# Optimization experiments

Measured on AMD Instinct MI355X. Metric: run time of the kernel, lower is better.

## Reference

```python
import jax, jax.numpy as jnp
import numpy as np
from jax import lax

# fixed finite-difference kernels (HWIO)
KXN = jnp.asarray([[0., -1., 1.]], dtype=jnp.float32).reshape(1, 3, 1, 1)
KXP = jnp.asarray([[-1., 1., 0.]], dtype=jnp.float32).reshape(1, 3, 1, 1)
KYN = jnp.asarray([[1.], [-1.], [0.]], dtype=jnp.float32).reshape(3, 1, 1, 1)
KYP = jnp.asarray([[0.], [1.], [-1.]], dtype=jnp.float32).reshape(3, 1, 1, 1)


def conv2d(x, k):
    # NHWC input, HWIO kernel, SAME padding, stride 1
    return lax.conv_general_dilated(x, k, (1, 1), 'SAME',
                                    dimension_numbers=('NHWC', 'HWIO', 'NHWC'))


def setup_inputs() -> dict:
    key = jax.random.key(0)
    ks = jax.random.split(key, 11)
    B, H, W = 8, 512, 512
    return {
        'u': jax.random.normal(ks[0], (B, H, W, 1), jnp.float32),
        'image': jax.random.uniform(ks[1], (B, H, W, 1), jnp.float32),
        'conv_kernel_x': jax.random.normal(ks[2], (3, 3, 1, 32), jnp.float32) * 0.05,
        'conv_kernel_y': jax.random.normal(ks[3], (3, 3, 1, 32), jnp.float32) * 0.05,
        'sep_kernel_depthwise': jax.random.normal(ks[4], (3, 3, 1, 8), jnp.float32) * 0.05,
        'sep_kernel_pointwise': jax.random.normal(ks[5], (1, 1, 8, 8), jnp.float32) * 0.05,
        'conv_kernel_curve_0': jax.random.normal(ks[6], (5, 5, 1, 8), jnp.float32) * 0.05,
        'conv_kernel_curve_1': jax.random.normal(ks[7], (5, 5, 8, 8), jnp.float32) * 0.05,
        'conv_kernel_curve_2': jax.random.normal(ks[8], (3, 3, 8, 16), jnp.float32) * 0.05,
        'conv_kernel_smoother': jax.random.normal(ks[9], (5, 5, 1, 1), jnp.float32) * 0.05,
        'kappa_kernel': jax.random.normal(ks[10], (H, W, 1), jnp.float32) * 0.05,
    }


def reference(u, image, conv_kernel_x, conv_kernel_y, sep_kernel_depthwise,
              sep_kernel_pointwise, conv_kernel_curve_0, conv_kernel_curve_1,
              conv_kernel_curve_2, conv_kernel_smoother, kappa_kernel):
    # separable conv on the (fixed) image: in_ch=1 so depthwise == standard conv
    edges = conv2d(conv2d(image, sep_kernel_depthwise), sep_kernel_pointwise)
    edges = jnp.sum(jax.nn.relu(edges), axis=-1, keepdims=True)
    edges = jax.nn.soft_sign(edges)  # x / (1 + |x|)

    grad_edges_x = jnp.sum(jax.nn.relu(conv2d(edges, conv_kernel_x)), axis=-1, keepdims=True)
    grad_edges_y = jnp.sum(jax.nn.relu(conv2d(edges, conv_kernel_y)), axis=-1, keepdims=True)

    xp = conv2d(u, KXP)
    xn = conv2d(u, KXN)
    yp = conv2d(u, KYP)
    yn = conv2d(u, KYN)

    fxp = jax.nn.relu(grad_edges_x)
    fxn = -jax.nn.relu(-grad_edges_x)
    fyp = jax.nn.relu(grad_edges_y)
    fyn = -jax.nn.relu(-grad_edges_y)

    kappa = conv2d(conv2d(conv2d(u, conv_kernel_curve_0), conv_kernel_curve_1), conv_kernel_curve_2)
    kappa = jnp.sum(kappa, axis=-1, keepdims=True)
    kappa = kappa * kappa_kernel  # (H,W,1) broadcasts over batch
    kappa = conv2d(kappa, conv_kernel_smoother)

    return u + fxp * xp + fxn * xn + fyp * yp + fyn * yn + edges + kappa
```

## Files before the change

### kernel.cpp

```cpp
#include <hip/hip_runtime.h>
#include <cstddef>

#define HH 512
#define WW 512
#define BB 8
#define T  32

#define F0    256
#define KT0   1280
#define WS_NEEDED_BYTES ((size_t)4096 * 4)

typedef __attribute__((ext_vector_type(8))) short short8;
typedef __attribute__((ext_vector_type(4))) float float4v;

__device__ inline unsigned short f2bf(float f) {
  unsigned u = __builtin_bit_cast(unsigned, f);
  unsigned r = (u + 0x7FFFu + ((u >> 16) & 1u)) >> 16;
  return (unsigned short)r;
}
__device__ inline float bf2f(unsigned short h) {
  unsigned u = ((unsigned)h) << 16;
  return __builtin_bit_cast(float, u);
}

__global__ __launch_bounds__(256) void precompute_kernels(
    const float* __restrict__ kd,
    const float* __restrict__ kp,
    const float* __restrict__ k0,
    const float* __restrict__ k1,
    const float* __restrict__ k2,
    const float* __restrict__ kx,
    const float* __restrict__ ky,
    float* __restrict__ ws) {
  __shared__ float k9[648];
  __shared__ float k2s[72];
  __shared__ float kef[121];
  const int tid = threadIdx.x;

  for (int idx = tid; idx < 72; idx += 256) {
    int c = idx & 7, pq = idx >> 3;
    float s = 0.f;
    for (int c0 = 0; c0 < 8; ++c0) s = fmaf(kd[pq * 8 + c0], kp[c0 * 8 + c], s);
    ws[idx] = s;
  }
  for (int idx = tid; idx < 72; idx += 256) {
    int c1 = idx & 7, tv = idx >> 3;
    float s = 0.f;
    for (int c2 = 0; c2 < 16; ++c2) s += k2[(tv * 8 + c1) * 16 + c2];
    k2s[idx] = s;
  }
  for (int idx = tid; idx < 648; idx += 256) {
    int c1 = idx & 7;
    int ab = idx >> 3;
    int a = ab / 9, b = ab % 9;
    float s = 0.f;
    int plo = a > 4 ? a - 4 : 0, phi = a < 4 ? a : 4;
    int qlo = b > 4 ? b - 4 : 0, qhi = b < 4 ? b : 4;
    for (int p = plo; p <= phi; ++p)
      for (int q = qlo; q <= qhi; ++q) {
        int r = a - p, sx = b - q;
        const float* k0p = &k0[(p * 5 + q) * 8];
        const float* k1p = &k1[((r * 5 + sx) * 8) * 8 + c1];
        for (int c0 = 0; c0 < 8; ++c0) s = fmaf(k0p[c0], k1p[c0 * 8], s);
      }
    k9[idx] = s;
  }
  for (int idx = tid; idx < 2048; idx += 256) {
    int nt = idx >> 9, ln = (idx >> 3) & 63, j = idx & 7;
    int k = (ln >> 4) * 8 + j;
    int n = nt * 16 + (ln & 15);
    float v = 0.f;
    if (k < 9) v = (n < 32) ? kx[k * 32 + n] : ky[k * 32 + (n - 32)];
    ((unsigned short*)ws)[F0 * 2 + idx] = f2bf(v);
  }
  __syncthreads();
  for (int idx = tid; idx < 121; idx += 256) {
    int A = idx / 11, B = idx % 11;
    float s = 0.f;
    int tlo = A > 8 ? A - 8 : 0, thi = A < 2 ? A : 2;
    int vlo = B > 8 ? B - 8 : 0, vhi = B < 2 ? B : 2;
    for (int t = tlo; t <= thi; ++t)
      for (int v = vlo; v <= vhi; ++v) {
        int a = A - t, b = B - v;
        for (int c1 = 0; c1 < 8; ++c1)
          s = fmaf(k9[(a * 9 + b) * 8 + c1], k2s[(t * 3 + v) * 8 + c1], s);
      }
    ws[72 + idx] = s;
    kef[idx] = s;
  }
  __syncthreads();
  for (int idx = tid; idx < 5632; idx += 256) {
    int b = idx >> 9, ln = (idx >> 3) & 63, j = idx & 7;
    int m = ln & 15;
    int k = (ln >> 4) * 8 + j;
    int a = k - m - 3;
    float v = ((unsigned)a < 11u) ? kef[a * 11 + b] : 0.f;
    ((unsigned short*)ws)[KT0 * 2 + idx] = f2bf(v);
  }
}

__global__ __launch_bounds__(256) void fused(
    const float* __restrict__ u, const float* __restrict__ img,
    const float* __restrict__ kk, const float* __restrict__ sm,
    const float* __restrict__ ws, float* __restrict__ out) {
  __shared__ unsigned short suT[58 * 72];
  __shared__ float si[36 * 36];
  __shared__ unsigned short sebf[34 * 36];
  __shared__ float skp[36 * 37];
  __shared__ float sgx[32 * 32];
  __shared__ float sgy[32 * 32];

  const int bx = blockIdx.x * T, by = blockIdx.y * T, b = blockIdx.z;
  const int tid = threadIdx.x;
  const float* ub = u + (size_t)b * HH * WW;
  const float* ib = img + (size_t)b * HH * WW;

  const int lane = tid & 63;
  const int wv   = tid >> 6;
  const int q    = lane >> 4;
  const int m    = lane & 15;

  for (int idx = tid; idx < 58 * 64; idx += 256) {
    int c = idx >> 6, r = idx & 63;
    int gy = by - 10 + r, gx = bx - 7 + c;
    float v = 0.f;
    if ((unsigned)gy < HH && (unsigned)gx < WW) v = ub[gy * WW + gx];
    suT[c * 72 + r] = f2bf(v);
  }
  for (int idx = tid; idx < 36 * 36; idx += 256) {
    int i = idx / 36, j = idx % 36;
    int gy = by - 2 + i, gx = bx - 2 + j;
    float v = 0.f;
    if ((unsigned)gy < HH && (unsigned)gx < WW) v = ib[gy * WW + gx];
    si[i * 36 + j] = v;
  }
  __syncthreads();

  for (int idx = tid; idx < 34 * 9; idx += 256) {
    int i = idx / 9, j0 = (idx % 9) * 4;
    float acc[8][4];
    #pragma unroll
    for (int c = 0; c < 8; ++c)
      #pragma unroll
      for (int t = 0; t < 4; ++t) acc[c][t] = 0.f;
    #pragma unroll
    for (int p = 0; p < 3; ++p) {
      float r[6];
      #pragma unroll
      for (int t = 0; t < 6; ++t) r[t] = si[(i + p) * 36 + j0 + t];
      #pragma unroll
      for (int qq = 0; qq < 3; ++qq) {
        float4 w0 = *reinterpret_cast<const float4*>(&ws[(p * 3 + qq) * 8]);
        float4 w1 = *reinterpret_cast<const float4*>(&ws[(p * 3 + qq) * 8 + 4]);
        #pragma unroll
        for (int t = 0; t < 4; ++t) {
          float v = r[qq + t];
          acc[0][t] = fmaf(v, w0.x, acc[0][t]);
          acc[1][t] = fmaf(v, w0.y, acc[1][t]);
          acc[2][t] = fmaf(v, w0.z, acc[2][t]);
          acc[3][t] = fmaf(v, w0.w, acc[3][t]);
          acc[4][t] = fmaf(v, w1.x, acc[4][t]);
          acc[5][t] = fmaf(v, w1.y, acc[5][t]);
          acc[6][t] = fmaf(v, w1.z, acc[6][t]);
          acc[7][t] = fmaf(v, w1.w, acc[7][t]);
        }
      }
    }
    int gy = by - 1 + i;
    #pragma unroll
    for (int t = 0; t < 4; ++t) {
      int j = j0 + t;
      if (j < 34) {
        int gx = bx - 1 + j;
        float val = 0.f;
        if ((unsigned)gy < HH && (unsigned)gx < WW) {
          float e = 0.f;
          #pragma unroll
          for (int c = 0; c < 8; ++c) e += fmaxf(acc[c][t], 0.f);
          val = e / (1.f + e);
        }
        sebf[i * 36 + j] = f2bf(val);
      }
    }
  }

  {
    const unsigned short* KT = ((const unsigned short*)ws) + KT0 * 2;
    for (int s = wv; s < 9; s += 4) {
      int sty = s / 3, stx = s % 3;
      float4v acc = {0.f, 0.f, 0.f, 0.f};
      #pragma unroll
      for (int bb = 0; bb < 11; ++bb) {
        short8 af = *reinterpret_cast<const short8*>(KT + (bb * 64 + lane) * 8);
        short8 bf = *reinterpret_cast<const short8*>(
            &suT[(stx * 16 + m + bb) * 72 + sty * 16 + q * 8]);
        acc = __builtin_amdgcn_mfma_f32_16x16x32_bf16(af, bf, acc, 0, 0, 0);
      }
      #pragma unroll
      for (int i = 0; i < 4; ++i) {
        int rl = sty * 16 + q * 4 + i, cl = stx * 16 + m;
        if (rl < 36 && cl < 36) {
          int yy = by - 2 + rl, xx = bx - 2 + cl;
          float v = 0.f;
          if ((unsigned)yy < HH && (unsigned)xx < WW)
            v = acc[i] * kk[(size_t)yy * WW + xx];
          skp[rl * 37 + cl] = v;
        }
      }
    }
  }
  __syncthreads();

  {
    short8 afr[4];
    const unsigned short* F = ((const unsigned short*)ws) + F0 * 2;
    #pragma unroll
    for (int t = 0; t < 4; ++t)
      afr[t] = *reinterpret_cast<const short8*>(F + (t * 64 + lane) * 8);

    #pragma unroll
    for (int h = 0; h < 32; h += 16) {
      const int cl = h + m;
      unsigned short W[9];
      #pragma unroll
      for (int d = 0; d < 3; ++d) {
        const unsigned short* rp = &sebf[(wv * 8 + d) * 36 + cl];
        W[3 * d + 0] = rp[0]; W[3 * d + 1] = rp[1]; W[3 * d + 2] = rp[2];
      }

      #pragma unroll
      for (int r = 0; r < 8; ++r) {
        short8 bv = (short8)0;
        if (q == 0) {
          #pragma unroll
          for (int j = 0; j < 8; ++j) bv[j] = (short)W[j];
        } else if (q == 1) {
          bv[0] = (short)W[8];
        }

        float4v c0 = {0.f, 0.f, 0.f, 0.f}, c1 = c0, c2 = c0, c3 = c0;
        c0 = __builtin_amdgcn_mfma_f32_16x16x32_bf16(afr[0], bv, c0, 0, 0, 0);
        c1 = __builtin_amdgcn_mfma_f32_16x16x32_bf16(afr[1], bv, c1, 0, 0, 0);
        c2 = __builtin_amdgcn_mfma_f32_16x16x32_bf16(afr[2], bv, c2, 0, 0, 0);
        c3 = __builtin_amdgcn_mfma_f32_16x16x32_bf16(afr[3], bv, c3, 0, 0, 0);

        float rx = 0.f, ry = 0.f;
        #pragma unroll
        for (int i = 0; i < 4; ++i) {
          rx += fmaxf(c0[i], 0.f) + fmaxf(c1[i], 0.f);
          ry += fmaxf(c2[i], 0.f) + fmaxf(c3[i], 0.f);
        }
        rx += __shfl_xor(rx, 16); rx += __shfl_xor(rx, 32);
        ry += __shfl_xor(ry, 16); ry += __shfl_xor(ry, 32);

        if (q == 0) {
          sgx[(wv * 8 + r) * 32 + cl] = rx;
          sgy[(wv * 8 + r) * 32 + cl] = ry;
        }

        if (r < 7) {
          #pragma unroll
          for (int t = 0; t < 6; ++t) W[t] = W[t + 3];
          const unsigned short* rp = &sebf[(wv * 8 + r + 3) * 36 + cl];
          W[6] = rp[0]; W[7] = rp[1]; W[8] = rp[2];
        }
      }
    }
  }
  __syncthreads();

  {
    const int oy = tid >> 3, ox = (tid & 7) * 4;
    const int gy = by + oy, gx = bx + ox;

    float4 gx4 = *reinterpret_cast<const float4*>(&sgx[oy * 32 + ox]);
    float4 gy4 = *reinterpret_cast<const float4*>(&sgy[oy * 32 + ox]);
    float gxa[4] = {gx4.x, gx4.y, gx4.z, gx4.w};
    float gya[4] = {gy4.x, gy4.y, gy4.z, gy4.w};

    float kap[4] = {0.f, 0.f, 0.f, 0.f};
    #pragma unroll
    for (int m5 = 0; m5 < 5; ++m5) {
      const float* row = &skp[(oy + m5) * 37 + ox];
      float r[8];
      #pragma unroll
      for (int t = 0; t < 8; ++t) r[t] = row[t];
      #pragma unroll
      for (int n = 0; n < 5; ++n) {
        float w = sm[m5 * 5 + n];
        #pragma unroll
        for (int t = 0; t < 4; ++t) kap[t] = fmaf(r[t + n], w, kap[t]);
      }
    }

    const float* ur = ub + (size_t)gy * WW + gx;
    float4 uc4 = *reinterpret_cast<const float4*>(ur);
    int jm = gx > 0 ? -1 : 0;
    float ul = ur[jm];
    ul = gx > 0 ? ul : 0.f;
    int ryd = gy < HH - 1 ? gy + 1 : HH - 1;
    float md = gy < HH - 1 ? 1.f : 0.f;
    float4 ud4 = *reinterpret_cast<const float4*>(ub + (size_t)ryd * WW + gx);

    float uc[4]  = {uc4.x, uc4.y, uc4.z, uc4.w};
    float ulx[4] = {ul, uc4.x, uc4.y, uc4.z};
    float udn[4] = {ud4.x * md, ud4.y * md, ud4.z * md, ud4.w * md};

    float res[4];
    #pragma unroll
    for (int t = 0; t < 4; ++t) {
      float xp = uc[t] - ulx[t];
      float yp = uc[t] - udn[t];
      float ec = bf2f(sebf[(oy + 1) * 36 + ox + 1 + t]);
      res[t] = uc[t] + gxa[t] * xp + gya[t] * yp + ec + kap[t];
    }
    *reinterpret_cast<float4*>(&out[((size_t)b * HH + gy) * WW + gx]) =
        make_float4(res[0], res[1], res[2], res[3]);
  }
}

__global__ __launch_bounds__(256) void forcing_main(
    const float* __restrict__ u, const float* __restrict__ img,
    const float* __restrict__ kx, const float* __restrict__ ky,
    const float* __restrict__ sm, const float* __restrict__ kk,
    const float* __restrict__ ws, float* __restrict__ out) {
  __shared__ float su[46][48];
  __shared__ float si[36][37];
  __shared__ float se[34][35];
  __shared__ float sk[36][37];
  __shared__ float w_edge[72];
  __shared__ float w_kx[288];
  __shared__ float w_ky[288];
  __shared__ float w_k11[124];
  __shared__ float w_sm[28];

  const int bx = blockIdx.x * T;
  const int by = blockIdx.y * T;
  const int b  = blockIdx.z;
  const int tid = threadIdx.x;
  const float* ub = u   + (size_t)b * HH * WW;
  const float* ib = img + (size_t)b * HH * WW;

  for (int i = tid; i < 72; i += 256)  w_edge[i] = ws[i];
  for (int i = tid; i < 121; i += 256) w_k11[i]  = ws[72 + i];
  for (int i = tid; i < 288; i += 256) { w_kx[i] = kx[i]; w_ky[i] = ky[i]; }
  if (tid < 25) w_sm[tid] = sm[tid];

  for (int idx = tid; idx < 46 * 46; idx += 256) {
    int i = idx / 46, j = idx % 46;
    int gy = by - 7 + i, gx = bx - 7 + j;
    float v = 0.f;
    if ((unsigned)gy < HH && (unsigned)gx < WW) v = ub[gy * WW + gx];
    su[i][j] = v;
  }
  for (int idx = tid; idx < 36 * 36; idx += 256) {
    int i = idx / 36, j = idx % 36;
    int gy = by - 2 + i, gx = bx - 2 + j;
    float v = 0.f;
    if ((unsigned)gy < HH && (unsigned)gx < WW) v = ib[gy * WW + gx];
    si[i][j] = v;
  }
  __syncthreads();

  for (int idx = tid; idx < 34 * 9; idx += 256) {
    int i = idx / 9, j0 = (idx % 9) * 4;
    float acc[8][4];
    #pragma unroll
    for (int c = 0; c < 8; ++c)
      #pragma unroll
      for (int t = 0; t < 4; ++t) acc[c][t] = 0.f;
    #pragma unroll
    for (int p = 0; p < 3; ++p) {
      float r[6];
      #pragma unroll
      for (int t = 0; t < 6; ++t) r[t] = si[i + p][j0 + t];
      #pragma unroll
      for (int q = 0; q < 3; ++q) {
        const float4 w0 = *reinterpret_cast<const float4*>(&w_edge[(p * 3 + q) * 8]);
        const float4 w1 = *reinterpret_cast<const float4*>(&w_edge[(p * 3 + q) * 8 + 4]);
        #pragma unroll
        for (int t = 0; t < 4; ++t) {
          float v = r[q + t];
          acc[0][t] = fmaf(v, w0.x, acc[0][t]);
          acc[1][t] = fmaf(v, w0.y, acc[1][t]);
          acc[2][t] = fmaf(v, w0.z, acc[2][t]);
          acc[3][t] = fmaf(v, w0.w, acc[3][t]);
          acc[4][t] = fmaf(v, w1.x, acc[4][t]);
          acc[5][t] = fmaf(v, w1.y, acc[5][t]);
          acc[6][t] = fmaf(v, w1.z, acc[6][t]);
          acc[7][t] = fmaf(v, w1.w, acc[7][t]);
        }
      }
    }
    int gy = by - 1 + i;
    #pragma unroll
    for (int t = 0; t < 4; ++t) {
      int j = j0 + t;
      if (j < 34) {
        int gx = bx - 1 + j;
        float val = 0.f;
        if ((unsigned)gy < HH && (unsigned)gx < WW) {
          float e = 0.f;
          #pragma unroll
          for (int c = 0; c < 8; ++c) e += fmaxf(acc[c][t], 0.f);
          val = e / (1.f + e);
        }
        se[i][j] = val;
      }
    }
  }

  for (int idx = tid; idx < 36 * 9; idx += 256) {
    int i = idx / 9, js = (idx % 9) * 4;
    float o0 = 0.f, o1 = 0.f, o2 = 0.f, o3 = 0.f;
    #pragma unroll
    for (int A = 0; A < 11; ++A) {
      const float* row = &su[i + A][js];
      float4 v0 = *reinterpret_cast<const float4*>(row);
      float4 v1 = *reinterpret_cast<const float4*>(row + 4);
      float4 v2 = *reinterpret_cast<const float4*>(row + 8);
      float r[14] = {v0.x, v0.y, v0.z, v0.w, v1.x, v1.y, v1.z, v1.w,
                     v2.x, v2.y, v2.z, v2.w, row[12], row[13]};
      #pragma unroll
      for (int B2 = 0; B2 < 11; ++B2) {
        float w = w_k11[A * 11 + B2];
        o0 = fmaf(r[B2],     w, o0);
        o1 = fmaf(r[B2 + 1], w, o1);
        o2 = fmaf(r[B2 + 2], w, o2);
        o3 = fmaf(r[B2 + 3], w, o3);
      }
    }
    int gy = by - 2 + i;
    float o[4] = {o0, o1, o2, o3};
    #pragma unroll
    for (int t = 0; t < 4; ++t) {
      int gx = bx - 2 + js + t;
      float val = 0.f;
      if ((unsigned)gy < HH && (unsigned)gx < WW) val = o[t] * kk[gy * WW + gx];
      sk[i][js + t] = val;
    }
  }
  __syncthreads();

  {
    const int oy = tid >> 3;
    const int ox = (tid & 7) * 4;
    const int gy = by + oy;
    const int gx = bx + ox;

    float e[3][6];
    #pragma unroll
    for (int p = 0; p < 3; ++p)
      #pragma unroll
      for (int t = 0; t < 6; ++t) e[p][t] = se[oy + p][ox + t];

    const float4* wx4 = reinterpret_cast<const float4*>(w_kx);
    const float4* wy4 = reinterpret_cast<const float4*>(w_ky);

    float gxa[4] = {0.f, 0.f, 0.f, 0.f};
    float gya[4] = {0.f, 0.f, 0.f, 0.f};
    #pragma unroll
    for (int cq = 0; cq < 8; ++cq) {
      float sx[4][4], sy[4][4];
      #pragma unroll
      for (int cc = 0; cc < 4; ++cc)
        #pragma unroll
        for (int t = 0; t < 4; ++t) { sx[cc][t] = 0.f; sy[cc][t] = 0.f; }
      #pragma unroll
      for (int p = 0; p < 3; ++p)
        #pragma unroll
        for (int q = 0; q < 3; ++q) {
          float4 wx = wx4[(p * 3 + q) * 8 + cq];
          float4 wy = wy4[(p * 3 + q) * 8 + cq];
          #pragma unroll
          for (int t = 0; t < 4; ++t) {
            float evv = e[p][q + t];
            sx[0][t] = fmaf(evv, wx.x, sx[0][t]);
            sx[1][t] = fmaf(evv, wx.y, sx[1][t]);
            sx[2][t] = fmaf(evv, wx.z, sx[2][t]);
            sx[3][t] = fmaf(evv, wx.w, sx[3][t]);
            sy[0][t] = fmaf(evv, wy.x, sy[0][t]);
            sy[1][t] = fmaf(evv, wy.y, sy[1][t]);
            sy[2][t] = fmaf(evv, wy.z, sy[2][t]);
            sy[3][t] = fmaf(evv, wy.w, sy[3][t]);
          }
        }
      #pragma unroll
      for (int cc = 0; cc < 4; ++cc)
        #pragma unroll
        for (int t = 0; t < 4; ++t) {
          gxa[t] += fmaxf(sx[cc][t], 0.f);
          gya[t] += fmaxf(sy[cc][t], 0.f);
        }
    }

    float res[4];
    #pragma unroll
    for (int t = 0; t < 4; ++t) {
      float kap = 0.f;
      #pragma unroll
      for (int m = 0; m < 5; ++m)
        #pragma unroll
        for (int n = 0; n < 5; ++n)
          kap = fmaf(sk[oy + m][ox + t + n], w_sm[m * 5 + n], kap);

      float uc = su[oy + 7][ox + 7 + t];
      float xp = uc - su[oy + 7][ox + 6 + t];
      float yp = uc - su[oy + 8][ox + 7 + t];
      float ec = se[oy + 1][ox + 1 + t];
      res[t] = uc + gxa[t] * xp + gya[t] * yp + ec + kap;
    }

    float4 r4 = make_float4(res[0], res[1], res[2], res[3]);
    *reinterpret_cast<float4*>(&out[((size_t)b * HH + gy) * WW + gx]) = r4;
  }
}

extern "C" void kernel_launch(void* const* d_in, const int* in_sizes, int n_in,
                              void* d_out, int out_size, void* d_ws, size_t ws_size,
                              hipStream_t stream) {
  const float* u   = (const float*)d_in[0];
  const float* img = (const float*)d_in[1];
  const float* kx  = (const float*)d_in[2];
  const float* ky  = (const float*)d_in[3];
  const float* kd  = (const float*)d_in[4];
  const float* kp  = (const float*)d_in[5];
  const float* k0  = (const float*)d_in[6];
  const float* k1  = (const float*)d_in[7];
  const float* k2  = (const float*)d_in[8];
  const float* sm  = (const float*)d_in[9];
  const float* kk  = (const float*)d_in[10];
  float* out = (float*)d_out;
  float* ws  = (float*)d_ws;

  precompute_kernels<<<1, 256, 0, stream>>>(kd, kp, k0, k1, k2, kx, ky, ws);
  dim3 grid(WW / T, HH / T, BB);
  if (ws != nullptr && ws_size >= WS_NEEDED_BYTES) {
    fused<<<grid, 256, 0, stream>>>(u, img, kk, sm, ws, out);
  } else {
    forcing_main<<<grid, 256, 0, stream>>>(u, img, kx, ky, sm, kk, ws, out);
  }
}
```

Baseline: 152.5 us.

## Fuse final epilogue into MFMA gradient loop, dropping sgx/sgy shared buffers

The gradient-force results stay in registers instead of going through shared memory. Each lane then computes the smoother convolution and the output for two rows of its column inside the MFMA loop, which removes a __syncthreads and two shared arrays. The u tile load loop is also reordered so consecutive threads read consecutive columns, giving coalesced global reads but scattered transposed LDS writes. The trade-offs are scalar rather than float4 global loads and stores, redundant skp reads, and more register pressure.

```diff
diff --git a/kernel.cpp b/kernel.cpp
--- a/kernel.cpp
+++ b/kernel.cpp
@@ -107,8 +107,6 @@
   __shared__ float si[36 * 36];
   __shared__ unsigned short sebf[34 * 36];
   __shared__ float skp[36 * 37];
-  __shared__ float sgx[32 * 32];
-  __shared__ float sgy[32 * 32];
 
   const int bx = blockIdx.x * T, by = blockIdx.y * T, b = blockIdx.z;
   const int tid = threadIdx.x;
@@ -120,8 +118,8 @@
   const int q    = lane >> 4;
   const int m    = lane & 15;
 
-  for (int idx = tid; idx < 58 * 64; idx += 256) {
-    int c = idx >> 6, r = idx & 63;
+  for (int idx = tid; idx < 64 * 58; idx += 256) {
+    int r = idx / 58, c = idx % 58;
     int gy = by - 10 + r, gx = bx - 7 + c;
     float v = 0.f;
     if ((unsigned)gy < HH && (unsigned)gx < WW) v = ub[gy * WW + gx];
@@ -228,6 +226,7 @@
         W[3 * d + 0] = rp[0]; W[3 * d + 1] = rp[1]; W[3 * d + 2] = rp[2];
       }
 
+      float rxv[8], ryv[8];
       #pragma unroll
       for (int r = 0; r < 8; ++r) {
         short8 bv = (short8)0;
@@ -252,11 +251,7 @@
         }
         rx += __shfl_xor(rx, 16); rx += __shfl_xor(rx, 32);
         ry += __shfl_xor(ry, 16); ry += __shfl_xor(ry, 32);
-
-        if (q == 0) {
-          sgx[(wv * 8 + r) * 32 + cl] = rx;
-          sgy[(wv * 8 + r) * 32 + cl] = ry;
-        }
+        rxv[r] = rx; ryv[r] = ry;
 
         if (r < 7) {
           #pragma unroll
@@ -265,57 +260,40 @@
           W[6] = rp[0]; W[7] = rp[1]; W[8] = rp[2];
         }
       }
-    }
-  }
-  __syncthreads();
-
-  {
-    const int oy = tid >> 3, ox = (tid & 7) * 4;
-    const int gy = by + oy, gx = bx + ox;
-
-    float4 gx4 = *reinterpret_cast<const float4*>(&sgx[oy * 32 + ox]);
-    float4 gy4 = *reinterpret_cast<const float4*>(&sgy[oy * 32 + ox]);
-    float gxa[4] = {gx4.x, gx4.y, gx4.z, gx4.w};
-    float gya[4] = {gy4.x, gy4.y, gy4.z, gy4.w};
-
-    float kap[4] = {0.f, 0.f, 0.f, 0.f};
-    #pragma unroll
-    for (int m5 = 0; m5 < 5; ++m5) {
-      const float* row = &skp[(oy + m5) * 37 + ox];
-      float r[8];
-      #pragma unroll
-      for (int t = 0; t < 8; ++t) r[t] = row[t];
-      #pragma unroll
-      for (int n = 0; n < 5; ++n) {
-        float w = sm[m5 * 5 + n];
-        #pragma unroll
-        for (int t = 0; t < 4; ++t) kap[t] = fmaf(r[t + n], w, kap[t]);
-      }
-    }
-
-    const float* ur = ub + (size_t)gy * WW + gx;
-    float4 uc4 = *reinterpret_cast<const float4*>(ur);
-    int jm = gx > 0 ? -1 : 0;
-    float ul = ur[jm];
-    ul = gx > 0 ? ul : 0.f;
-    int ryd = gy < HH - 1 ? gy + 1 : HH - 1;
-    float md = gy < HH - 1 ? 1.f : 0.f;
-    float4 ud4 = *reinterpret_cast<const float4*>(ub + (size_t)ryd * WW + gx);
-
-    float uc[4]  = {uc4.x, uc4.y, uc4.z, uc4.w};
-    float ulx[4] = {ul, uc4.x, uc4.y, uc4.z};
-    float udn[4] = {ud4.x * md, ud4.y * md, ud4.z * md, ud4.w * md};
-
-    float res[4];
-    #pragma unroll
-    for (int t = 0; t < 4; ++t) {
-      float xp = uc[t] - ulx[t];
-      float yp = uc[t] - udn[t];
-      float ec = bf2f(sebf[(oy + 1) * 36 + ox + 1 + t]);
-      res[t] = uc[t] + gxa[t] * xp + gya[t] * yp + ec + kap[t];
-    }
-    *reinterpret_cast<float4*>(&out[((size_t)b * HH + gy) * WW + gx]) =
-        make_float4(res[0], res[1], res[2], res[3]);
+
+      {
+        const int row0 = wv * 8 + 2 * q;
+        const int gx = bx + cl;
+        float sk6[6][5];
+        #pragma unroll
+        for (int rr = 0; rr < 6; ++rr)
+          #pragma unroll
+          for (int n = 0; n < 5; ++n)
+            sk6[rr][n] = skp[(row0 + rr) * 37 + cl + n];
+
+        #pragma unroll
+        for (int s = 0; s < 2; ++s) {
+          int oy = row0 + s;
+          int gy = by + oy;
+          float kap = 0.f;
+          #pragma unroll
+          for (int m5 = 0; m5 < 5; ++m5)
+            #pragma unroll
+            for (int n = 0; n < 5; ++n)
+              kap = fmaf(sk6[s + m5][n], sm[m5 * 5 + n], kap);
+
+          float ec = bf2f(sebf[(oy + 1) * 36 + cl + 1]);
+          const float* ur = ub + (size_t)gy * WW + gx;
+          float uc = ur[0];
+          float ul = gx > 0 ? ur[-1] : 0.f;
+          float ud = gy < HH - 1 ? ur[WW] : 0.f;
+          float xp = uc - ul;
+          float yp = uc - ud;
+          out[((size_t)b * HH + gy) * WW + gx] =
+              uc + rxv[2 * q + s] * xp + ryv[2 * q + s] * yp + ec + kap;
+        }
+      }
+    }
   }
 }
 
```

Measured after the change: 148.2 us. -2.8%, faster.
